# Performance work log

Hardware: AMD Instinct MI355X
Metric: run time of the kernel (lower is better)

The kernel has to match this reference:

```python
import jax, jax.numpy as jnp
import numpy as np

DT = 10.0 / 200  # 0.05
DX = 20.0 / 128  # 0.15625

# 5x5 fixed finite-difference stencils (torch Conv2d = cross-correlation, so use as-is)
_LAPL = np.array([[0, 0, -1/12, 0, 0],
                  [0, 0,  4/3,  0, 0],
                  [-1/12, 4/3, -5, 4/3, -1/12],
                  [0, 0,  4/3,  0, 0],
                  [0, 0, -1/12, 0, 0]], dtype=np.float32)
_PAR_X = np.array([[0, 0,  1/12, 0, 0],
                   [0, 0, -8/12, 0, 0],
                   [0, 0,  0,    0, 0],
                   [0, 0,  8/12, 0, 0],
                   [0, 0, -1/12, 0, 0]], dtype=np.float32)


def _conv2d_valid(x, kern):
    # x: [N, 1, H, W], kern: [5, 5] -> [N, 1, H-4, W-4]
    return jax.lax.conv_general_dilated(x, jnp.asarray(kern)[None, None], (1, 1), 'VALID')


def _time_deriv(x):
    # x: [T, B, 1, h, w]; central diff interior, one-sided at endpoints (all /DT)
    interior = (x[2:] - x[:-2]) / (2.0 * DT)
    t0 = (-1.5 * x[0] + 2.0 * x[1] - 0.5 * x[2]) / DT
    tn = (0.5 * x[-3] - 2.0 * x[-2] + 1.5 * x[-1]) / DT
    return jnp.concatenate([t0[None], interior, tn[None]], axis=0)


def setup_inputs() -> dict:
    key = jax.random.key(0)
    output = jax.random.normal(key, (20, 8, 3, 256, 256), dtype=jnp.float32)
    return {"output": output}


def reference(output):
    T, B, C, H, W = output.shape
    u = output[:, :, 1:2]  # [T,B,1,H,W]
    v = output[:, :, 2:3]

    lap_u = _conv2d_valid(u.reshape(T * B, 1, H, W), _LAPL).reshape(T, B, 1, H - 4, W - 4) / (DX ** 2)
    lap_v = _conv2d_valid(v.reshape(T * B, 1, H, W), _LAPL).reshape(T, B, 1, H - 4, W - 4) / (DX ** 2)

    uc = u[:, :, :, 2:-2, 2:-2]  # [T,B,1,H-4,W-4]
    vc = v[:, :, :, 2:-2, 2:-2]
    u_t = _time_deriv(uc)
    v_t = _time_deriv(vc)

    Du, Dv = 0.16, 0.08
    f, k = 0.06, 0.062
    f_u = Du * lap_u - uc * vc ** 2 + f * (1.0 - uc) - u_t
    f_v = Dv * lap_v + uc * vc ** 2 - (f + k) * vc - v_t
    return (f_u, f_v)
```

## Files before the change

### kernel.cpp

```cpp
#include <hip/hip_runtime.h>


#define T_OUT (8 * 252 * 252)

typedef float vf4 __attribute__((ext_vector_type(4)));

static __device__ __forceinline__ vf4 lds4u(const float* p) {
    vf4 v;
    __builtin_memcpy(&v, p, 16);
    return v;
}

#define GS_INT(c) { \
    float ut = (ucn.c - u_cm1.c) * hdt; \
    float vt = (vcn.c - v_cm1.c) * hdt; \
    float uvv = u_cc.c * v_cc.c * v_cc.c; \
    fu.c = Du * u_lm1.c - uvv + fR * (1.0f - u_cc.c) - ut; \
    fv.c = Dv * v_lm1.c + uvv - (fR + kR) * v_cc.c - vt; }

#define GS_T0(c) { \
    float ut = (-1.5f * u_cm1.c + 2.0f * u_cc.c - 0.5f * ucn.c) * inv_dt; \
    float vt = (-1.5f * v_cm1.c + 2.0f * v_cc.c - 0.5f * vcn.c) * inv_dt; \
    float uvv = u_cm1.c * v_cm1.c * v_cm1.c; \
    fu.c = Du * u_l0.c - uvv + fR * (1.0f - u_cm1.c) - ut; \
    fv.c = Dv * v_l0.c + uvv - (fR + kR) * v_cm1.c - vt; }

#define GS_TN(c) { \
    float ut = (0.5f * u_cm2.c - 2.0f * u_cm1.c + 1.5f * u_cc.c) * inv_dt; \
    float vt = (0.5f * v_cm2.c - 2.0f * v_cm1.c + 1.5f * v_cc.c) * inv_dt; \
    float uvv = u_cc.c * v_cc.c * v_cc.c; \
    fu.c = Du * u_lm1.c - uvv + fR * (1.0f - u_cc.c) - ut; \
    fv.c = Dv * v_lm1.c + uvv - (fR + kR) * v_cc.c - vt; }

#define ISSUE(t) { \
    const float* bt = base0 + (size_t)(t) * tStride; \
    sreg0 = *(const vf4*)(bt + (size_t)(y0 + w) * 256 + col); \
    sreg1 = *(const vf4*)(bt + (size_t)(y0 + w + 4) * 256 + col); \
    sreg2 = *(const vf4*)(bt + planeStride + (size_t)(y0 + w) * 256 + col); \
    sreg3 = *(const vf4*)(bt + planeStride + (size_t)(y0 + w + 4) * 256 + col); }

__global__ __launch_bounds__(256) void gs_loss_kernel(
    const float* __restrict__ in, float* __restrict__ out)
{
    __shared__ float lds[2][16][256];

    const int tid = threadIdx.x;
    const int w   = tid >> 6;
    const int ln  = tid & 63;

    const int b     = blockIdx.x & 7;
    const int ytile = blockIdx.x >> 3;
    const int y0    = ytile * 4;

    const int planeStride = 256 * 256;
    const int bStride     = 3 * planeStride;
    const int tStride     = 24 * planeStride;

    const int col = ln * 4;
    const float* base0 = in + (size_t)b * bStride + planeStride;

    const int yloc = w;
    const int xg   = ln;
    const int x0   = xg * 4;
    const bool active = (xg < 63);

    const int total = 20 * T_OUT;
    float* outu = out + ((size_t)b * 252 + (y0 + yloc)) * 252 + x0;
    float* outv = outu + total;

    const float C1 = 4.0f / 3.0f, C2 = 1.0f / 12.0f;
    const float inv_dx2 = 1.0f / (0.15625f * 0.15625f);
    const float inv_dt  = 20.0f;
    const float hdt     = 10.0f;
    const float Du = 0.16f, Dv = 0.08f, fR = 0.06f, kR = 0.062f;

    vf4 u_cm2{}, u_cm1{}, u_cc{}, u_lm1{}, u_l0{};
    vf4 v_cm2{}, v_cm1{}, v_cc{}, v_lm1{}, v_l0{};

    vf4 sreg0, sreg1, sreg2, sreg3;
    ISSUE(0);

#pragma unroll
    for (int t = 0; t < 20; ++t) {
        float (*L)[256] = lds[t & 1];

        *(vf4*)&L[w     ][col] = sreg0;
        *(vf4*)&L[w + 4 ][col] = sreg1;
        *(vf4*)&L[w + 8 ][col] = sreg2;
        *(vf4*)&L[w + 12][col] = sreg3;

        __syncthreads();

        if (t < 19) ISSUE(t + 1);

        if (active) {
            vf4 uL  = *(const vf4*)&L[yloc + 2][x0];
            vf4 uR  = *(const vf4*)&L[yloc + 2][x0 + 4];
            vf4 um1 = lds4u(&L[yloc + 1][x0 + 2]);
            vf4 up1 = lds4u(&L[yloc + 3][x0 + 2]);
            vf4 um2 = lds4u(&L[yloc    ][x0 + 2]);
            vf4 up2 = lds4u(&L[yloc + 4][x0 + 2]);

            vf4 vL  = *(const vf4*)&L[yloc + 10][x0];
            vf4 vR  = *(const vf4*)&L[yloc + 10][x0 + 4];
            vf4 vm1 = lds4u(&L[yloc +  9][x0 + 2]);
            vf4 vp1 = lds4u(&L[yloc + 11][x0 + 2]);
            vf4 vm2 = lds4u(&L[yloc +  8][x0 + 2]);
            vf4 vp2 = lds4u(&L[yloc + 12][x0 + 2]);

            vf4 lu, lv;
            lu.x = (C1*(uL.y + uL.w + um1.x + up1.x) - C2*(uL.x + uR.x + um2.x + up2.x) - 5.0f*uL.z) * inv_dx2;
            lu.y = (C1*(uL.z + uR.x + um1.y + up1.y) - C2*(uL.y + uR.y + um2.y + up2.y) - 5.0f*uL.w) * inv_dx2;
            lu.z = (C1*(uL.w + uR.y + um1.z + up1.z) - C2*(uL.z + uR.z + um2.z + up2.z) - 5.0f*uR.x) * inv_dx2;
            lu.w = (C1*(uR.x + uR.z + um1.w + up1.w) - C2*(uL.w + uR.w + um2.w + up2.w) - 5.0f*uR.y) * inv_dx2;
            lv.x = (C1*(vL.y + vL.w + vm1.x + vp1.x) - C2*(vL.x + vR.x + vm2.x + vp2.x) - 5.0f*vL.z) * inv_dx2;
            lv.y = (C1*(vL.z + vR.x + vm1.y + vp1.y) - C2*(vL.y + vR.y + vm2.y + vp2.y) - 5.0f*vL.w) * inv_dx2;
            lv.z = (C1*(vL.w + vR.y + vm1.z + vp1.z) - C2*(vL.z + vR.z + vm2.z + vp2.z) - 5.0f*vR.x) * inv_dx2;
            lv.w = (C1*(vR.x + vR.z + vm1.w + vp1.w) - C2*(vL.w + vR.w + vm2.w + vp2.w) - 5.0f*vR.y) * inv_dx2;

            vf4 ucn = {uL.z, uL.w, uR.x, uR.y};
            vf4 vcn = {vL.z, vL.w, vR.x, vR.y};

            if (t == 0) { u_l0 = lu; v_l0 = lv; }

            if (t == 2) {
                vf4 fu, fv;
                GS_T0(x); GS_T0(y); GS_T0(z); GS_T0(w);
                __builtin_nontemporal_store(fu, (vf4*)(outu));
                __builtin_nontemporal_store(fv, (vf4*)(outv));
            }

            if (t >= 2) {
                vf4 fu, fv;
                GS_INT(x); GS_INT(y); GS_INT(z); GS_INT(w);
                __builtin_nontemporal_store(fu, (vf4*)(outu + (size_t)(t - 1) * T_OUT));
                __builtin_nontemporal_store(fv, (vf4*)(outv + (size_t)(t - 1) * T_OUT));
            }

            u_cm2 = u_cm1; u_cm1 = u_cc; u_cc = ucn; u_lm1 = lu;
            v_cm2 = v_cm1; v_cm1 = v_cc; v_cc = vcn; v_lm1 = lv;
        }
    }

    if (active) {
        vf4 fu, fv;
        GS_TN(x); GS_TN(y); GS_TN(z); GS_TN(w);
        __builtin_nontemporal_store(fu, (vf4*)(outu + (size_t)19 * T_OUT));
        __builtin_nontemporal_store(fv, (vf4*)(outv + (size_t)19 * T_OUT));
    }
}

extern "C" void kernel_launch(void* const* d_in, const int* in_sizes, int n_in,
                              void* d_out, int out_size, void* d_ws, size_t ws_size,
                              hipStream_t stream) {
    const float* in = (const float*)d_in[0];
    float* out = (float*)d_out;

    gs_loss_kernel<<<8 * 63, 256, 0, stream>>>(in, out);
}
```

Before: 191.0 us.

## Compute two output rows per thread and prefetch two timesteps ahead

Each block now covers 8 output rows instead of 4, and each thread computes two rows, which shrinks the halo overhead from 8/4 to 12/8 loaded rows per output row. The grid drops from 504 to 256 blocks. Global loads are double-buffered in registers (A/B sets) so the loads for t+2 are issued while step t computes, deepening the prefetch. The costs are more registers (launch_bounds(256,1)), a larger LDS buffer and fewer blocks to spread across the GPU's CUs, which may lower occupancy.

```diff
diff --git a/kernel.cpp b/kernel.cpp
--- a/kernel.cpp
+++ b/kernel.cpp
@@ -11,143 +11,194 @@
     return v;
 }
 
+struct GSRow {
+    vf4 u_cm2, u_cm1, u_cc, u_lm1, u_l0;
+    vf4 v_cm2, v_cm1, v_cc, v_lm1, v_l0;
+};
+
 #define GS_INT(c) { \
-    float ut = (ucn.c - u_cm1.c) * hdt; \
-    float vt = (vcn.c - v_cm1.c) * hdt; \
-    float uvv = u_cc.c * v_cc.c * v_cc.c; \
-    fu.c = Du * u_lm1.c - uvv + fR * (1.0f - u_cc.c) - ut; \
-    fv.c = Dv * v_lm1.c + uvv - (fR + kR) * v_cc.c - vt; }
+    float ut = (ucn.c - s.u_cm1.c) * hdt; \
+    float vt = (vcn.c - s.v_cm1.c) * hdt; \
+    float uvv = s.u_cc.c * s.v_cc.c * s.v_cc.c; \
+    fu.c = Du * s.u_lm1.c - uvv + fR * (1.0f - s.u_cc.c) - ut; \
+    fv.c = Dv * s.v_lm1.c + uvv - (fR + kR) * s.v_cc.c - vt; }
 
 #define GS_T0(c) { \
-    float ut = (-1.5f * u_cm1.c + 2.0f * u_cc.c - 0.5f * ucn.c) * inv_dt; \
-    float vt = (-1.5f * v_cm1.c + 2.0f * v_cc.c - 0.5f * vcn.c) * inv_dt; \
-    float uvv = u_cm1.c * v_cm1.c * v_cm1.c; \
-    fu.c = Du * u_l0.c - uvv + fR * (1.0f - u_cm1.c) - ut; \
-    fv.c = Dv * v_l0.c + uvv - (fR + kR) * v_cm1.c - vt; }
+    float ut = (-1.5f * s.u_cm1.c + 2.0f * s.u_cc.c - 0.5f * ucn.c) * inv_dt; \
+    float vt = (-1.5f * s.v_cm1.c + 2.0f * s.v_cc.c - 0.5f * vcn.c) * inv_dt; \
+    float uvv = s.u_cm1.c * s.v_cm1.c * s.v_cm1.c; \
+    fu.c = Du * s.u_l0.c - uvv + fR * (1.0f - s.u_cm1.c) - ut; \
+    fv.c = Dv * s.v_l0.c + uvv - (fR + kR) * s.v_cm1.c - vt; }
 
 #define GS_TN(c) { \
-    float ut = (0.5f * u_cm2.c - 2.0f * u_cm1.c + 1.5f * u_cc.c) * inv_dt; \
-    float vt = (0.5f * v_cm2.c - 2.0f * v_cm1.c + 1.5f * v_cc.c) * inv_dt; \
-    float uvv = u_cc.c * v_cc.c * v_cc.c; \
-    fu.c = Du * u_lm1.c - uvv + fR * (1.0f - u_cc.c) - ut; \
-    fv.c = Dv * v_lm1.c + uvv - (fR + kR) * v_cc.c - vt; }
-
-#define ISSUE(t) { \
-    const float* bt = base0 + (size_t)(t) * tStride; \
-    sreg0 = *(const vf4*)(bt + (size_t)(y0 + w) * 256 + col); \
-    sreg1 = *(const vf4*)(bt + (size_t)(y0 + w + 4) * 256 + col); \
-    sreg2 = *(const vf4*)(bt + planeStride + (size_t)(y0 + w) * 256 + col); \
-    sreg3 = *(const vf4*)(bt + planeStride + (size_t)(y0 + w + 4) * 256 + col); }
-
-__global__ __launch_bounds__(256) void gs_loss_kernel(
-    const float* __restrict__ in, float* __restrict__ out)
+    float ut = (0.5f * s.u_cm2.c - 2.0f * s.u_cm1.c + 1.5f * s.u_cc.c) * inv_dt; \
+    float vt = (0.5f * s.v_cm2.c - 2.0f * s.v_cm1.c + 1.5f * s.v_cc.c) * inv_dt; \
+    float uvv = s.u_cc.c * s.v_cc.c * s.v_cc.c; \
+    fu.c = Du * s.u_lm1.c - uvv + fR * (1.0f - s.u_cc.c) - ut; \
+    fv.c = Dv * s.v_lm1.c + uvv - (fR + kR) * s.v_cc.c - vt; }
+
+static __device__ __forceinline__ void gs_step(
+    const float (*L)[256], int R, int x0, int t, GSRow& s, bool act,
+    float* __restrict__ outu, float* __restrict__ outv)
 {
-    __shared__ float lds[2][16][256];
-
-    const int tid = threadIdx.x;
-    const int w   = tid >> 6;
-    const int ln  = tid & 63;
-
-    const int b     = blockIdx.x & 7;
-    const int ytile = blockIdx.x >> 3;
-    const int y0    = ytile * 4;
-
-    const int planeStride = 256 * 256;
-    const int bStride     = 3 * planeStride;
-    const int tStride     = 24 * planeStride;
-
-    const int col = ln * 4;
-    const float* base0 = in + (size_t)b * bStride + planeStride;
-
-    const int yloc = w;
-    const int xg   = ln;
-    const int x0   = xg * 4;
-    const bool active = (xg < 63);
-
-    const int total = 20 * T_OUT;
-    float* outu = out + ((size_t)b * 252 + (y0 + yloc)) * 252 + x0;
-    float* outv = outu + total;
-
     const float C1 = 4.0f / 3.0f, C2 = 1.0f / 12.0f;
     const float inv_dx2 = 1.0f / (0.15625f * 0.15625f);
     const float inv_dt  = 20.0f;
     const float hdt     = 10.0f;
     const float Du = 0.16f, Dv = 0.08f, fR = 0.06f, kR = 0.062f;
 
-    vf4 u_cm2{}, u_cm1{}, u_cc{}, u_lm1{}, u_l0{};
-    vf4 v_cm2{}, v_cm1{}, v_cc{}, v_lm1{}, v_l0{};
-
-    vf4 sreg0, sreg1, sreg2, sreg3;
-    ISSUE(0);
+    vf4 uL  = *(const vf4*)&L[R + 2][x0];
+    vf4 uR  = *(const vf4*)&L[R + 2][x0 + 4];
+    vf4 um1 = lds4u(&L[R + 1][x0 + 2]);
+    vf4 up1 = lds4u(&L[R + 3][x0 + 2]);
+    vf4 um2 = lds4u(&L[R    ][x0 + 2]);
+    vf4 up2 = lds4u(&L[R + 4][x0 + 2]);
+
+    vf4 vL  = *(const vf4*)&L[R + 14][x0];
+    vf4 vR  = *(const vf4*)&L[R + 14][x0 + 4];
+    vf4 vm1 = lds4u(&L[R + 13][x0 + 2]);
+    vf4 vp1 = lds4u(&L[R + 15][x0 + 2]);
+    vf4 vm2 = lds4u(&L[R + 12][x0 + 2]);
+    vf4 vp2 = lds4u(&L[R + 16][x0 + 2]);
+
+    vf4 lu, lv;
+    lu.x = (C1*(uL.y + uL.w + um1.x + up1.x) - C2*(uL.x + uR.x + um2.x + up2.x) - 5.0f*uL.z) * inv_dx2;
+    lu.y = (C1*(uL.z + uR.x + um1.y + up1.y) - C2*(uL.y + uR.y + um2.y + up2.y) - 5.0f*uL.w) * inv_dx2;
+    lu.z = (C1*(uL.w + uR.y + um1.z + up1.z) - C2*(uL.z + uR.z + um2.z + up2.z) - 5.0f*uR.x) * inv_dx2;
+    lu.w = (C1*(uR.x + uR.z + um1.w + up1.w) - C2*(uL.w + uR.w + um2.w + up2.w) - 5.0f*uR.y) * inv_dx2;
+    lv.x = (C1*(vL.y + vL.w + vm1.x + vp1.x) - C2*(vL.x + vR.x + vm2.x + vp2.x) - 5.0f*vL.z) * inv_dx2;
+    lv.y = (C1*(vL.z + vR.x + vm1.y + vp1.y) - C2*(vL.y + vR.y + vm2.y + vp2.y) - 5.0f*vL.w) * inv_dx2;
+    lv.z = (C1*(vL.w + vR.y + vm1.z + vp1.z) - C2*(vL.z + vR.z + vm2.z + vp2.z) - 5.0f*vR.x) * inv_dx2;
+    lv.w = (C1*(vR.x + vR.z + vm1.w + vp1.w) - C2*(vL.w + vR.w + vm2.w + vp2.w) - 5.0f*vR.y) * inv_dx2;
+
+    vf4 ucn = {uL.z, uL.w, uR.x, uR.y};
+    vf4 vcn = {vL.z, vL.w, vR.x, vR.y};
+
+    if (t == 0) { s.u_l0 = lu; s.v_l0 = lv; }
+
+    if (t == 2 && act) {
+        vf4 fu, fv;
+        GS_T0(x); GS_T0(y); GS_T0(z); GS_T0(w);
+        __builtin_nontemporal_store(fu, (vf4*)(outu));
+        __builtin_nontemporal_store(fv, (vf4*)(outv));
+    }
+
+    if (t >= 2 && act) {
+        vf4 fu, fv;
+        GS_INT(x); GS_INT(y); GS_INT(z); GS_INT(w);
+        __builtin_nontemporal_store(fu, (vf4*)(outu + (size_t)(t - 1) * T_OUT));
+        __builtin_nontemporal_store(fv, (vf4*)(outv + (size_t)(t - 1) * T_OUT));
+    }
+
+    s.u_cm2 = s.u_cm1; s.u_cm1 = s.u_cc; s.u_cc = ucn; s.u_lm1 = lu;
+    s.v_cm2 = s.v_cm1; s.v_cm1 = s.v_cc; s.v_cc = vcn; s.v_lm1 = lv;
+}
+
+static __device__ __forceinline__ void gs_tail(
+    GSRow& s, bool act, float* __restrict__ outu, float* __restrict__ outv)
+{
+    const float inv_dt = 20.0f;
+    const float Du = 0.16f, Dv = 0.08f, fR = 0.06f, kR = 0.062f;
+    if (!act) return;
+    vf4 fu, fv;
+    GS_TN(x); GS_TN(y); GS_TN(z); GS_TN(w);
+    __builtin_nontemporal_store(fu, (vf4*)(outu + (size_t)19 * T_OUT));
+    __builtin_nontemporal_store(fv, (vf4*)(outv + (size_t)19 * T_OUT));
+}
+
+__global__ __launch_bounds__(256, 1) void gs_loss_kernel(
+    const float* __restrict__ in, float* __restrict__ out)
+{
+    __shared__ float lds[2][24][256];
+
+    const int tid = threadIdx.x;
+    const int w   = tid >> 6;
+    const int ln  = tid & 63;
+
+    const int b     = blockIdx.x & 7;
+    const int ytile = blockIdx.x >> 3;
+    const int y0    = ytile * 8;
+
+    const int planeStride = 256 * 256;
+    const int bStride     = 3 * planeStride;
+    const int tStride     = 24 * planeStride;
+
+    const int col = ln * 4;
+    const float* base0 = in + (size_t)b * bStride + planeStride;
+
+    const int gr0 = y0 + w;
+    const int gr1 = (y0 + w + 4 < 256) ? (y0 + w + 4) : 255;
+    const int gr2 = (y0 + w + 8 < 256) ? (y0 + w + 8) : 255;
+    const size_t r0 = (size_t)gr0 * 256 + col;
+    const size_t r1 = (size_t)gr1 * 256 + col;
+    const size_t r2 = (size_t)gr2 * 256 + col;
+
+    const int x0 = ln * 4;
+    const bool active = (ln < 63);
+    const bool act2   = active && (y0 + w + 4 < 252);
+
+    const int total = 20 * T_OUT;
+    float* outu1 = out + ((size_t)b * 252 + (y0 + w)) * 252 + x0;
+    float* outv1 = outu1 + total;
+    const int y2 = act2 ? (y0 + w + 4) : (y0 + w);
+    float* outu2 = out + ((size_t)b * 252 + y2) * 252 + x0;
+    float* outv2 = outu2 + total;
+
+    GSRow s1{}, s2{};
+
+    vf4 sA0, sA1, sA2, sA3, sA4, sA5;
+    vf4 sB0, sB1, sB2, sB3, sB4, sB5;
+
+#define ISSUE_A(t) { const float* bt = base0 + (size_t)(t) * tStride; \
+    sA0 = *(const vf4*)(bt + r0); \
+    sA1 = *(const vf4*)(bt + r1); \
+    sA2 = *(const vf4*)(bt + r2); \
+    sA3 = *(const vf4*)(bt + planeStride + r0); \
+    sA4 = *(const vf4*)(bt + planeStride + r1); \
+    sA5 = *(const vf4*)(bt + planeStride + r2); }
+#define ISSUE_B(t) { const float* bt = base0 + (size_t)(t) * tStride; \
+    sB0 = *(const vf4*)(bt + r0); \
+    sB1 = *(const vf4*)(bt + r1); \
+    sB2 = *(const vf4*)(bt + r2); \
+    sB3 = *(const vf4*)(bt + planeStride + r0); \
+    sB4 = *(const vf4*)(bt + planeStride + r1); \
+    sB5 = *(const vf4*)(bt + planeStride + r2); }
+
+    ISSUE_A(0);
+    ISSUE_B(1);
 
 #pragma unroll
     for (int t = 0; t < 20; ++t) {
         float (*L)[256] = lds[t & 1];
 
-        *(vf4*)&L[w     ][col] = sreg0;
-        *(vf4*)&L[w + 4 ][col] = sreg1;
-        *(vf4*)&L[w + 8 ][col] = sreg2;
-        *(vf4*)&L[w + 12][col] = sreg3;
+        if ((t & 1) == 0) {
+            *(vf4*)&L[w     ][col] = sA0;
+            *(vf4*)&L[w + 4 ][col] = sA1;
+            *(vf4*)&L[w + 8 ][col] = sA2;
+            *(vf4*)&L[w + 12][col] = sA3;
+            *(vf4*)&L[w + 16][col] = sA4;
+            *(vf4*)&L[w + 20][col] = sA5;
+        } else {
+            *(vf4*)&L[w     ][col] = sB0;
+            *(vf4*)&L[w + 4 ][col] = sB1;
+            *(vf4*)&L[w + 8 ][col] = sB2;
+            *(vf4*)&L[w + 12][col] = sB3;
+            *(vf4*)&L[w + 16][col] = sB4;
+            *(vf4*)&L[w + 20][col] = sB5;
+        }
 
         __syncthreads();
 
-        if (t < 19) ISSUE(t + 1);
-
-        if (active) {
-            vf4 uL  = *(const vf4*)&L[yloc + 2][x0];
-            vf4 uR  = *(const vf4*)&L[yloc + 2][x0 + 4];
-            vf4 um1 = lds4u(&L[yloc + 1][x0 + 2]);
-            vf4 up1 = lds4u(&L[yloc + 3][x0 + 2]);
-            vf4 um2 = lds4u(&L[yloc    ][x0 + 2]);
-            vf4 up2 = lds4u(&L[yloc + 4][x0 + 2]);
-
-            vf4 vL  = *(const vf4*)&L[yloc + 10][x0];
-            vf4 vR  = *(const vf4*)&L[yloc + 10][x0 + 4];
-            vf4 vm1 = lds4u(&L[yloc +  9][x0 + 2]);
-            vf4 vp1 = lds4u(&L[yloc + 11][x0 + 2]);
-            vf4 vm2 = lds4u(&L[yloc +  8][x0 + 2]);
-            vf4 vp2 = lds4u(&L[yloc + 12][x0 + 2]);
-
-            vf4 lu, lv;
-            lu.x = (C1*(uL.y + uL.w + um1.x + up1.x) - C2*(uL.x + uR.x + um2.x + up2.x) - 5.0f*uL.z) * inv_dx2;
-            lu.y = (C1*(uL.z + uR.x + um1.y + up1.y) - C2*(uL.y + uR.y + um2.y + up2.y) - 5.0f*uL.w) * inv_dx2;
-            lu.z = (C1*(uL.w + uR.y + um1.z + up1.z) - C2*(uL.z + uR.z + um2.z + up2.z) - 5.0f*uR.x) * inv_dx2;
-            lu.w = (C1*(uR.x + uR.z + um1.w + up1.w) - C2*(uL.w + uR.w + um2.w + up2.w) - 5.0f*uR.y) * inv_dx2;
-            lv.x = (C1*(vL.y + vL.w + vm1.x + vp1.x) - C2*(vL.x + vR.x + vm2.x + vp2.x) - 5.0f*vL.z) * inv_dx2;
-            lv.y = (C1*(vL.z + vR.x + vm1.y + vp1.y) - C2*(vL.y + vR.y + vm2.y + vp2.y) - 5.0f*vL.w) * inv_dx2;
-            lv.z = (C1*(vL.w + vR.y + vm1.z + vp1.z) - C2*(vL.z + vR.z + vm2.z + vp2.z) - 5.0f*vR.x) * inv_dx2;
-            lv.w = (C1*(vR.x + vR.z + vm1.w + vp1.w) - C2*(vL.w + vR.w + vm2.w + vp2.w) - 5.0f*vR.y) * inv_dx2;
-
-            vf4 ucn = {uL.z, uL.w, uR.x, uR.y};
-            vf4 vcn = {vL.z, vL.w, vR.x, vR.y};
-
-            if (t == 0) { u_l0 = lu; v_l0 = lv; }
-
-            if (t == 2) {
-                vf4 fu, fv;
-                GS_T0(x); GS_T0(y); GS_T0(z); GS_T0(w);
-                __builtin_nontemporal_store(fu, (vf4*)(outu));
-                __builtin_nontemporal_store(fv, (vf4*)(outv));
-            }
-
-            if (t >= 2) {
-                vf4 fu, fv;
-                GS_INT(x); GS_INT(y); GS_INT(z); GS_INT(w);
-                __builtin_nontemporal_store(fu, (vf4*)(outu + (size_t)(t - 1) * T_OUT));
-                __builtin_nontemporal_store(fv, (vf4*)(outv + (size_t)(t - 1) * T_OUT));
-            }
-
-            u_cm2 = u_cm1; u_cm1 = u_cc; u_cc = ucn; u_lm1 = lu;
-            v_cm2 = v_cm1; v_cm1 = v_cc; v_cc = vcn; v_lm1 = lv;
+        if (t + 2 < 20) {
+            if ((t & 1) == 0) { ISSUE_A(t + 2); } else { ISSUE_B(t + 2); }
         }
+
+        gs_step(L, w,     x0, t, s1, active, outu1, outv1);
+        gs_step(L, w + 4, x0, t, s2, act2,   outu2, outv2);
     }
 
-    if (active) {
-        vf4 fu, fv;
-        GS_TN(x); GS_TN(y); GS_TN(z); GS_TN(w);
-        __builtin_nontemporal_store(fu, (vf4*)(outu + (size_t)19 * T_OUT));
-        __builtin_nontemporal_store(fv, (vf4*)(outv + (size_t)19 * T_OUT));
-    }
+    gs_tail(s1, active, outu1, outv1);
+    gs_tail(s2, act2,   outu2, outv2);
 }
 
 extern "C" void kernel_launch(void* const* d_in, const int* in_sizes, int n_in,
@@ -156,5 +207,5 @@
     const float* in = (const float*)d_in[0];
     float* out = (float*)d_out;
 
-    gs_loss_kernel<<<8 * 63, 256, 0, stream>>>(in, out);
-}
+    gs_loss_kernel<<<8 * 32, 256, 0, stream>>>(in, out);
+}
```

Result: no change. 189.5 us (-0.8%).
